# Kernel tuning notes

Measured on AMD Instinct MI355X. Metric: run time of the kernel, lower is better.

## Reference

```python
import jax, jax.numpy as jnp
import numpy as np

S_CNT, R_CNT, P_CNT = 10000, 10000, 50000
K_S, K_R, K_P = 64, 64, 128
T = 50
N = 1_000_000


def setup_inputs() -> dict:
    key = jax.random.key(0)
    ks, kr, kp, kt, kws, kwr, kwp = jax.random.split(key, 7)
    s = jax.random.randint(ks, (N,), 0, S_CNT)
    r = jax.random.randint(kr, (N,), 0, R_CNT)
    p = jax.random.randint(kp, (N,), 0, P_CNT)
    t = jax.random.randint(kt, (N,), 0, T)
    X = jnp.stack([s, r, p, t], axis=1).astype(jnp.int64)  # n x 4
    # xavier_uniform-like init: bound = sqrt(6/(fan_in+fan_out))
    def xavier(k, shape):
        bound = np.sqrt(6.0 / (shape[0] + shape[1])).astype(np.float32)
        return jax.random.uniform(k, shape, jnp.float32, -bound, bound)
    s_embeds = xavier(kws, (T * S_CNT, K_S))
    r_embeds = xavier(kwr, (T * R_CNT, K_R))
    p_embeds = xavier(kwp, (P_CNT, K_P))
    return {"X": X, "s_embeds": s_embeds, "r_embeds": r_embeds, "p_embeds": p_embeds}


def reference(X, s_embeds, r_embeds, p_embeds):
    s, r, p, t = X[:, 0], X[:, 1], X[:, 2], X[:, 3]
    st = s + t * S_CNT
    rt = r + t * R_CNT
    se = s_embeds[st]            # [n, K_S]
    re = r_embeds[rt]            # [n, K_R]
    pe = p_embeds[p]             # [n, K_S + K_R]
    # dot(concat(se, re), pe) without materializing the concat
    prod = jnp.sum(se * pe[:, :K_S], axis=1) + jnp.sum(re * pe[:, K_S:], axis=1)
    return jax.nn.sigmoid(prod)  # [n]
```

## Files before the change

### kernel.cpp

```cpp
#include <hip/hip_runtime.h>
#include <cstdint>

#define S_CNT 10000
#define R_CNT 10000
#define PG 1024
#define PROWS 49
#define CAP 1216
#define SPLIT 2
#define PACKED_OFF_B 16384
#define WS_NEED ((size_t)PACKED_OFF_B + 16ull * PG * CAP)

__global__ __launch_bounds__(256) void zero_kernel(int4* __restrict__ cur4) {
    cur4[threadIdx.x] = make_int4(0, 0, 0, 0);
}

__global__ __launch_bounds__(256) void bin_kernel(
    const int* __restrict__ X, int n, int* __restrict__ cursors,
    int4* __restrict__ packed,
    const float* __restrict__ se, const float* __restrict__ re,
    const float* __restrict__ pe, float* __restrict__ out)
{
    __shared__ int lhist[PG], lbase[PG], lcur[PG];
    const int tid = threadIdx.x;
    const long long base = (long long)blockIdx.x * 1024;

    #pragma unroll
    for (int k = 0; k < PG / 256; ++k) lhist[tid + 256 * k] = 0;
    __syncthreads();

    int4 xs[4];
    int  grp[4];
    #pragma unroll
    for (int it = 0; it < 4; ++it) {
        const long long i = base + it * 256 + tid;
        if (i < n) {
            xs[it] = *reinterpret_cast<const int4*>(X + 4 * i);
            grp[it] = xs[it].z / PROWS;
            atomicAdd(&lhist[grp[it]], 1);
        } else grp[it] = -1;
    }
    __syncthreads();
    #pragma unroll
    for (int k = 0; k < PG / 256; ++k) {
        const int b = tid + 256 * k;
        const int c = lhist[b];
        lbase[b] = c ? atomicAdd(&cursors[b], c) : 0;
        lcur[b] = 0;
    }
    __syncthreads();
    #pragma unroll
    for (int it = 0; it < 4; ++it) {
        const int g = grp[it];
        if (g < 0) continue;
        const long long i = base + it * 256 + tid;
        const int rank = lbase[g] + atomicAdd(&lcur[g], 1);
        if (rank < CAP) {
            packed[(long long)g * CAP + rank] =
                make_int4(xs[it].x | (xs[it].w << 16), xs[it].y, xs[it].z, (int)i);
        } else {
            const long long st = (long long)xs[it].x + (long long)xs[it].w * S_CNT;
            const long long rt = (long long)xs[it].y + (long long)xs[it].w * R_CNT;
            const long long p  = xs[it].z;
            float acc = 0.f;
            for (int k = 0; k < 64; ++k)
                acc += se[st * 64 + k] * pe[p * 128 + k]
                     + re[rt * 64 + k] * pe[p * 128 + 64 + k];
            out[i] = 1.0f / (1.0f + __expf(-acc));
        }
    }
}

__global__ __launch_bounds__(256) void compute_kernel(
    const int* __restrict__ cursors, const int4* __restrict__ packed,
    const float* __restrict__ s_embeds, const float* __restrict__ r_embeds,
    const float* __restrict__ p_embeds, float* __restrict__ out)
{
    __shared__ __align__(16) float plds[PROWS * 128];
    const int g = blockIdx.x / SPLIT;
    const int q = blockIdx.x % SPLIT;
    const int cnt = min(cursors[g], CAP);
    if (cnt == 0) return;

    const int prow0 = g * PROWS;
    const int rows = min(PROWS, 50000 - prow0);
    const int nf4 = rows * 32;
    const float4* src = reinterpret_cast<const float4*>(p_embeds + (long long)prow0 * 128);
    for (int k = threadIdx.x; k < nf4; k += 256)
        reinterpret_cast<float4*>(plds)[k] = src[k];
    __syncthreads();

    const int lo  = (int)((long long)cnt * q / SPLIT);
    const int end = (int)((long long)cnt * (q + 1) / SPLIT);
    if (lo >= end) return;

    const int gl = threadIdx.x >> 4;
    const int l  = threadIdx.x & 15;
    const int4* pk = packed + (long long)g * CAP;

    for (int sb = lo; sb < end; sb += 32) {
        const int jA = sb + gl;
        const int jB = sb + 16 + gl;
        const int4 a = pk[min(jA, end - 1)];
        const int4 b = pk[min(jB, end - 1)];

        const int sA = a.x & 0xFFFF, tA = a.x >> 16;
        const int sB = b.x & 0xFFFF, tB = b.x >> 16;
        const int stA = sA + tA * S_CNT, rtA = a.y + tA * R_CNT;
        const int stB = sB + tB * S_CNT, rtB = b.y + tB * R_CNT;

        const float4 seA = *reinterpret_cast<const float4*>(s_embeds + (long long)stA * 64 + l * 4);
        const float4 reA = *reinterpret_cast<const float4*>(r_embeds + (long long)rtA * 64 + l * 4);
        const float4 seB = *reinterpret_cast<const float4*>(s_embeds + (long long)stB * 64 + l * 4);
        const float4 reB = *reinterpret_cast<const float4*>(r_embeds + (long long)rtB * 64 + l * 4);

        const int pA = (a.z - prow0) * 128;
        const int pB = (b.z - prow0) * 128;
        const float4 plA = *reinterpret_cast<const float4*>(plds + pA + l * 4);
        const float4 phA = *reinterpret_cast<const float4*>(plds + pA + 64 + l * 4);
        const float4 plB = *reinterpret_cast<const float4*>(plds + pB + l * 4);
        const float4 phB = *reinterpret_cast<const float4*>(plds + pB + 64 + l * 4);

        float accA = seA.x * plA.x + seA.y * plA.y + seA.z * plA.z + seA.w * plA.w
                   + reA.x * phA.x + reA.y * phA.y + reA.z * phA.z + reA.w * phA.w;
        float accB = seB.x * plB.x + seB.y * plB.y + seB.z * plB.z + seB.w * plB.w
                   + reB.x * phB.x + reB.y * phB.y + reB.z * phB.z + reB.w * phB.w;

        accA += __shfl_xor(accA, 1, 64);  accB += __shfl_xor(accB, 1, 64);
        accA += __shfl_xor(accA, 2, 64);  accB += __shfl_xor(accB, 2, 64);
        accA += __shfl_xor(accA, 4, 64);  accB += __shfl_xor(accB, 4, 64);
        accA += __shfl_xor(accA, 8, 64);  accB += __shfl_xor(accB, 8, 64);

        if (l == 0 && jA < end) out[a.w] = 1.0f / (1.0f + __expf(-accA));
        if (l == 0 && jB < end) out[b.w] = 1.0f / (1.0f + __expf(-accB));
    }
}

__global__ __launch_bounds__(256) void direct_kernel(
    const int* __restrict__ X,
    const float* __restrict__ s_embeds, const float* __restrict__ r_embeds,
    const float* __restrict__ p_embeds, float* __restrict__ out, int n) {
    const int g = threadIdx.x >> 4;
    const int l = threadIdx.x & 15;
    const int i = blockIdx.x * 16 + g;
    if (i >= n) return;
    const int4 xi = *reinterpret_cast<const int4*>(X + 4ll * i);
    const long long st = (long long)xi.x + (long long)xi.w * S_CNT;
    const long long rt = (long long)xi.y + (long long)xi.w * R_CNT;
    const long long p  = xi.z;
    const float4 se = *reinterpret_cast<const float4*>(s_embeds + st * 64 + l * 4);
    const float4 re = *reinterpret_cast<const float4*>(r_embeds + rt * 64 + l * 4);
    const float4 pl = *reinterpret_cast<const float4*>(p_embeds + p * 128 + l * 4);
    const float4 ph = *reinterpret_cast<const float4*>(p_embeds + p * 128 + 64 + l * 4);
    float acc = se.x * pl.x + se.y * pl.y + se.z * pl.z + se.w * pl.w
              + re.x * ph.x + re.y * ph.y + re.z * ph.z + re.w * ph.w;
    acc += __shfl_xor(acc, 1, 64);
    acc += __shfl_xor(acc, 2, 64);
    acc += __shfl_xor(acc, 4, 64);
    acc += __shfl_xor(acc, 8, 64);
    if (l == 0) out[i] = 1.0f / (1.0f + __expf(-acc));
}

extern "C" void kernel_launch(void* const* d_in, const int* in_sizes, int n_in,
                              void* d_out, int out_size, void* d_ws, size_t ws_size,
                              hipStream_t stream) {
    const int*   X        = (const int*)d_in[0];
    const float* s_embeds = (const float*)d_in[1];
    const float* r_embeds = (const float*)d_in[2];
    const float* p_embeds = (const float*)d_in[3];
    float* out = (float*)d_out;
    const int n = in_sizes[0] / 4;

    if (ws_size < WS_NEED) {
        direct_kernel<<<(n + 15) / 16, 256, 0, stream>>>(
            X, s_embeds, r_embeds, p_embeds, out, n);
        return;
    }

    int* cursors = (int*)d_ws;
    int4* packed = reinterpret_cast<int4*>((char*)d_ws + PACKED_OFF_B);

    zero_kernel<<<1, 256, 0, stream>>>(reinterpret_cast<int4*>(cursors));
    bin_kernel<<<(n + 1023) / 1024, 256, 0, stream>>>(
        X, n, cursors, packed, s_embeds, r_embeds, p_embeds, out);
    compute_kernel<<<PG * SPLIT, 256, 0, stream>>>(
        cursors, packed, s_embeds, r_embeds, p_embeds, out);
}
```

Measured before the change: 148.8 us.

## Drop LDS staging of p rows; use finer bins and read p_embeds via cache

The number of bins goes from 1024 to 2000, each covering 25 p rows, and the SPLIT scheme is removed, so each compute block handles one bin. The compute kernel no longer stages p_embeds rows into shared memory and reads them straight from global memory, counting on L2 locality within the bin. The bin kernel now stores precomputed st and rt indices in the packed entries, which saves the unpacking arithmetic, and the kernel adds occupancy hints. The trade-off is redundant global p reads in place of LDS reads, more bins, and a larger histogram in shared memory for the bin kernel.

```diff
diff --git a/kernel.cpp b/kernel.cpp
--- a/kernel.cpp
+++ b/kernel.cpp
@@ -3,15 +3,14 @@
 
 #define S_CNT 10000
 #define R_CNT 10000
-#define PG 1024
-#define PROWS 49
-#define CAP 1216
-#define SPLIT 2
+#define PG 2000
+#define PROWS 25
+#define CAP 634
 #define PACKED_OFF_B 16384
 #define WS_NEED ((size_t)PACKED_OFF_B + 16ull * PG * CAP)
 
 __global__ __launch_bounds__(256) void zero_kernel(int4* __restrict__ cur4) {
-    cur4[threadIdx.x] = make_int4(0, 0, 0, 0);
+    cur4[blockIdx.x * 256 + threadIdx.x] = make_int4(0, 0, 0, 0);
 }
 
 __global__ __launch_bounds__(256) void bin_kernel(
@@ -24,8 +23,7 @@
     const int tid = threadIdx.x;
     const long long base = (long long)blockIdx.x * 1024;
 
-    #pragma unroll
-    for (int k = 0; k < PG / 256; ++k) lhist[tid + 256 * k] = 0;
+    for (int k = tid; k < PG; k += 256) lhist[k] = 0;
     __syncthreads();
 
     int4 xs[4];
@@ -40,23 +38,23 @@
         } else grp[it] = -1;
     }
     __syncthreads();
-    #pragma unroll
-    for (int k = 0; k < PG / 256; ++k) {
-        const int b = tid + 256 * k;
-        const int c = lhist[b];
-        lbase[b] = c ? atomicAdd(&cursors[b], c) : 0;
-        lcur[b] = 0;
+    for (int k = tid; k < PG; k += 256) {
+        const int c = lhist[k];
+        lbase[k] = c ? atomicAdd(&cursors[k], c) : 0;
+        lcur[k] = 0;
     }
     __syncthreads();
     #pragma unroll
     for (int it = 0; it < 4; ++it) {
         const int g = grp[it];
         if (g < 0) continue;
-        const long long i = base + it * 256 + tid;
+        const int i = (int)(base + it * 256 + tid);
         const int rank = lbase[g] + atomicAdd(&lcur[g], 1);
         if (rank < CAP) {
             packed[(long long)g * CAP + rank] =
-                make_int4(xs[it].x | (xs[it].w << 16), xs[it].y, xs[it].z, (int)i);
+                make_int4(xs[it].x + xs[it].w * S_CNT,
+                          xs[it].y + xs[it].w * R_CNT,
+                          xs[it].z, i);
         } else {
             const long long st = (long long)xs[it].x + (long long)xs[it].w * S_CNT;
             const long long rt = (long long)xs[it].y + (long long)xs[it].w * R_CNT;
@@ -70,55 +68,34 @@
     }
 }
 
-__global__ __launch_bounds__(256) void compute_kernel(
+__global__ __launch_bounds__(256, 8) void compute_kernel(
     const int* __restrict__ cursors, const int4* __restrict__ packed,
     const float* __restrict__ s_embeds, const float* __restrict__ r_embeds,
     const float* __restrict__ p_embeds, float* __restrict__ out)
 {
-    __shared__ __align__(16) float plds[PROWS * 128];
-    const int g = blockIdx.x / SPLIT;
-    const int q = blockIdx.x % SPLIT;
+    const int g = blockIdx.x;
     const int cnt = min(cursors[g], CAP);
     if (cnt == 0) return;
-
-    const int prow0 = g * PROWS;
-    const int rows = min(PROWS, 50000 - prow0);
-    const int nf4 = rows * 32;
-    const float4* src = reinterpret_cast<const float4*>(p_embeds + (long long)prow0 * 128);
-    for (int k = threadIdx.x; k < nf4; k += 256)
-        reinterpret_cast<float4*>(plds)[k] = src[k];
-    __syncthreads();
-
-    const int lo  = (int)((long long)cnt * q / SPLIT);
-    const int end = (int)((long long)cnt * (q + 1) / SPLIT);
-    if (lo >= end) return;
 
     const int gl = threadIdx.x >> 4;
     const int l  = threadIdx.x & 15;
     const int4* pk = packed + (long long)g * CAP;
+    const int last = cnt - 1;
 
-    for (int sb = lo; sb < end; sb += 32) {
-        const int jA = sb + gl;
-        const int jB = sb + 16 + gl;
-        const int4 a = pk[min(jA, end - 1)];
-        const int4 b = pk[min(jB, end - 1)];
+    for (int sb = 0; sb < cnt; sb += 32) {
+        const int jA = sb + gl * 2;
+        const int jB = jA + 1;
+        const int4 a = pk[min(jA, last)];
+        const int4 b = pk[min(jB, last)];
 
-        const int sA = a.x & 0xFFFF, tA = a.x >> 16;
-        const int sB = b.x & 0xFFFF, tB = b.x >> 16;
-        const int stA = sA + tA * S_CNT, rtA = a.y + tA * R_CNT;
-        const int stB = sB + tB * S_CNT, rtB = b.y + tB * R_CNT;
-
-        const float4 seA = *reinterpret_cast<const float4*>(s_embeds + (long long)stA * 64 + l * 4);
-        const float4 reA = *reinterpret_cast<const float4*>(r_embeds + (long long)rtA * 64 + l * 4);
-        const float4 seB = *reinterpret_cast<const float4*>(s_embeds + (long long)stB * 64 + l * 4);
-        const float4 reB = *reinterpret_cast<const float4*>(r_embeds + (long long)rtB * 64 + l * 4);
-
-        const int pA = (a.z - prow0) * 128;
-        const int pB = (b.z - prow0) * 128;
-        const float4 plA = *reinterpret_cast<const float4*>(plds + pA + l * 4);
-        const float4 phA = *reinterpret_cast<const float4*>(plds + pA + 64 + l * 4);
-        const float4 plB = *reinterpret_cast<const float4*>(plds + pB + l * 4);
-        const float4 phB = *reinterpret_cast<const float4*>(plds + pB + 64 + l * 4);
+        const float4 seA = *reinterpret_cast<const float4*>(s_embeds + (unsigned)a.x * 64u + l * 4);
+        const float4 reA = *reinterpret_cast<const float4*>(r_embeds + (unsigned)a.y * 64u + l * 4);
+        const float4 seB = *reinterpret_cast<const float4*>(s_embeds + (unsigned)b.x * 64u + l * 4);
+        const float4 reB = *reinterpret_cast<const float4*>(r_embeds + (unsigned)b.y * 64u + l * 4);
+        const float4 plA = *reinterpret_cast<const float4*>(p_embeds + (unsigned)a.z * 128u + l * 4);
+        const float4 phA = *reinterpret_cast<const float4*>(p_embeds + (unsigned)a.z * 128u + 64u + l * 4);
+        const float4 plB = *reinterpret_cast<const float4*>(p_embeds + (unsigned)b.z * 128u + l * 4);
+        const float4 phB = *reinterpret_cast<const float4*>(p_embeds + (unsigned)b.z * 128u + 64u + l * 4);
 
         float accA = seA.x * plA.x + seA.y * plA.y + seA.z * plA.z + seA.w * plA.w
                    + reA.x * phA.x + reA.y * phA.y + reA.z * phA.z + reA.w * phA.w;
@@ -130,8 +107,10 @@
         accA += __shfl_xor(accA, 4, 64);  accB += __shfl_xor(accB, 4, 64);
         accA += __shfl_xor(accA, 8, 64);  accB += __shfl_xor(accB, 8, 64);
 
-        if (l == 0 && jA < end) out[a.w] = 1.0f / (1.0f + __expf(-accA));
-        if (l == 0 && jB < end) out[b.w] = 1.0f / (1.0f + __expf(-accB));
+        if (l == 0) {
+            if (jA <= last) out[a.w] = 1.0f / (1.0f + __expf(-accA));
+            if (jB <= last) out[b.w] = 1.0f / (1.0f + __expf(-accB));
+        }
     }
 }
 
@@ -179,9 +158,9 @@
     int* cursors = (int*)d_ws;
     int4* packed = reinterpret_cast<int4*>((char*)d_ws + PACKED_OFF_B);
 
-    zero_kernel<<<1, 256, 0, stream>>>(reinterpret_cast<int4*>(cursors));
+    zero_kernel<<<2, 256, 0, stream>>>(reinterpret_cast<int4*>(cursors));
     bin_kernel<<<(n + 1023) / 1024, 256, 0, stream>>>(
         X, n, cursors, packed, s_embeds, r_embeds, p_embeds, out);
-    compute_kernel<<<PG * SPLIT, 256, 0, stream>>>(
+    compute_kernel<<<PG, 256, 0, stream>>>(
         cursors, packed, s_embeds, r_embeds, p_embeds, out);
 }
```

Result: slower. 167.3 us (+12.4%).
